# Optimization experiments

Hardware: AMD Instinct MI355X
Metric: run time of the kernel (lower is better)

The kernel has to match this reference:

```python
import jax, jax.numpy as jnp
import numpy as np

D_MODEL = 1024
N_HEAD = 16
D_K = D_MODEL // N_HEAD
D_FF = 2048
EPS = 1e-6
SCALE = np.sqrt(D_K).astype(np.float32)


def layer_norm(x, alpha, beta):
    # Faithful to source: unbiased std (ddof=1), eps added to std
    mean = jnp.mean(x, axis=-1, keepdims=True)
    std = jnp.std(x, axis=-1, keepdims=True, ddof=1) + EPS
    return alpha * (x - mean) / std + beta


def setup_inputs() -> dict:
    key = jax.random.key(0)
    ks = jax.random.split(key, 12)
    s = 0.02
    return {
        "x": jax.random.normal(ks[0], (4, 1024, D_MODEL), dtype=jnp.float32),
        "Wq": jax.random.normal(ks[1], (D_MODEL, D_MODEL), dtype=jnp.float32) * s,
        "bq": jax.random.normal(ks[2], (D_MODEL,), dtype=jnp.float32) * s,
        "Wo": jax.random.normal(ks[3], (D_MODEL, D_MODEL), dtype=jnp.float32) * s,
        "bo": jax.random.normal(ks[4], (D_MODEL,), dtype=jnp.float32) * s,
        "W1": jax.random.normal(ks[5], (D_MODEL, D_FF), dtype=jnp.float32) * s,
        "b1": jax.random.normal(ks[6], (D_FF,), dtype=jnp.float32) * s,
        "W2": jax.random.normal(ks[7], (D_FF, D_MODEL), dtype=jnp.float32) * s,
        "b2": jax.random.normal(ks[8], (D_MODEL,), dtype=jnp.float32) * s,
        "alpha": jnp.ones((D_MODEL,), dtype=jnp.float32),
        "beta": jnp.ones((D_MODEL,), dtype=jnp.float32),
    }


def reference(x, Wq, bq, Wo, bo, W1, b1, W2, b2, alpha, beta):
    b, s, d = x.shape
    # Source bug kept: q, k, v all use q_linear
    def proj(t):
        return (t @ Wq + bq).reshape(b, s, N_HEAD, D_K).transpose(0, 2, 1, 3)
    q = proj(x)  # [b,h,s,dk]
    k = proj(x)
    v = proj(x)
    scores = jnp.einsum('bhqd,bhkd->bhqk', q, k) / SCALE
    scores = jax.nn.softmax(scores, axis=-1)
    z = jnp.einsum('bhqk,bhkd->bhqd', scores, v)
    concat = z.transpose(0, 2, 1, 3).reshape(b, s, d)
    attn_out = concat @ Wo + bo
    x = layer_norm(x + attn_out, alpha, beta)
    ff = jax.nn.relu(x @ W1 + b1) @ W2 + b2
    x = layer_norm(x + ff, alpha, beta)  # source reuses norm_1
    return x
```

## Files before the change

kernel.cpp:

```cpp
#include <hip/hip_runtime.h>
#include <hip/hip_bf16.h>
#include <stdint.h>

#define TOK   4096
#define DMODEL 1024
#define DFF    2048
#define NHEAD  16
#define DK     64

typedef unsigned short u16;
typedef __attribute__((ext_vector_type(8))) short short8;
typedef __attribute__((ext_vector_type(4))) float f32x4;

typedef __attribute__((address_space(1))) void gvoid;
typedef __attribute__((address_space(3))) void lvoid;

#define QSCALE   0.35355339f
#define QUNSCALE 2.82842712f

__device__ __forceinline__ u16 f2b(float f) {
    uint32_t x = __builtin_bit_cast(uint32_t, f);
    x += 0x7FFFu + ((x >> 16) & 1u);
    return (u16)(x >> 16);
}
__device__ __forceinline__ float b2f(u16 u) {
    uint32_t x = ((uint32_t)u) << 16;
    return __builtin_bit_cast(float, x);
}
__device__ __forceinline__ uint32_t f2b2(float lo, float hi) {
    return (uint32_t)f2b(lo) | ((uint32_t)f2b(hi) << 16);
}

__device__ __forceinline__ void gload16(const void* g, void* l) {
    __builtin_amdgcn_global_load_lds((gvoid*)g, (lvoid*)l, 16, 0, 0);
}

__device__ __forceinline__ void cvt_tr_dev(
    const float* __restrict__ W, u16* __restrict__ Wt, int K, int N,
    int bx, int by, int tid, u16 T[64][68])
{
    const int tx = tid & 15, ty = tid >> 4;
    const int n0 = bx * 64, k0 = by * 64;
#pragma unroll
    for (int i = 0; i < 4; i++) {
        int k = ty + i * 16;
        float4 v = *(const float4*)&W[(size_t)(k0 + k) * N + n0 + tx * 4];
        T[tx * 4 + 0][k] = f2b(v.x);
        T[tx * 4 + 1][k] = f2b(v.y);
        T[tx * 4 + 2][k] = f2b(v.z);
        T[tx * 4 + 3][k] = f2b(v.w);
    }
    __syncthreads();
#pragma unroll
    for (int i = 0; i < 4; i++) {
        int n = ty + i * 16;
        ushort4 o;
        o.x = T[n][tx * 4 + 0]; o.y = T[n][tx * 4 + 1];
        o.z = T[n][tx * 4 + 2]; o.w = T[n][tx * 4 + 3];
        *(ushort4*)&Wt[(size_t)(n0 + n) * K + k0 + tx * 4] = o;
    }
}

__global__ __launch_bounds__(256) void prep_all(
    const float* __restrict__ Wq, const float* __restrict__ Wo,
    const float* __restrict__ W1, const float* __restrict__ W2,
    u16* __restrict__ Wqt, u16* __restrict__ Wot,
    u16* __restrict__ W1t, u16* __restrict__ W2t,
    const float* __restrict__ x, u16* __restrict__ xb)
{
    __shared__ u16 T[64][68];
    const int id = blockIdx.x, tid = threadIdx.x;
    if (id < 256) {
        cvt_tr_dev(Wq, Wqt, 1024, 1024, id & 15, id >> 4, tid, T);
    } else if (id < 512) {
        int t = id - 256;
        cvt_tr_dev(Wo, Wot, 1024, 1024, t & 15, t >> 4, tid, T);
    } else if (id < 1024) {
        int t = id - 512;
        cvt_tr_dev(W1, W1t, 1024, 2048, t & 31, t >> 5, tid, T);
    } else if (id < 1536) {
        int t = id - 1024;
        cvt_tr_dev(W2, W2t, 2048, 1024, t & 15, t >> 4, tid, T);
    } else {
        size_t base = (size_t)(id - 1536) * 1024 + tid;
#pragma unroll
        for (int j = 0; j < 4; j++) {
            float4 v = ((const float4*)x)[base + j * 256];
            ((uint2*)xb)[base + j * 256] =
                make_uint2(f2b2(v.x, v.y), f2b2(v.z, v.w));
        }
    }
}

template<int BM, int BN, bool RELU, bool OUTBF16, bool QOUT>
__global__ __launch_bounds__(256) void gemm_mfma(
    const u16* __restrict__ A, const u16* __restrict__ Bt,
    const float* __restrict__ bias, void* __restrict__ Cv,
    u16* __restrict__ CT, float oscale,
    int M, int N, int K)
{
    constexpr int MF = BM / 32;
    constexpr int NF = BN / 32;
    constexpr int ASTR = BM * 64;
    constexpr int BSTR = BN * 64;
    static_assert(MF + NF == 6, "vmcnt immediates assume 6 loads/tile");
    __shared__ __align__(16) u16 As[2 * ASTR];
    __shared__ __align__(16) u16 Bs[2 * BSTR];

    const int tid  = threadIdx.x;
    const int lane = tid & 63;
    const int wid  = tid >> 6;
    const int wm = wid >> 1, wn = wid & 1;
    const int frow = lane & 15, fk = lane >> 4;

    const int gx = N / BN;
    const int gy = M / BM;
    const int rpx = gy >> 3;
    const int L = blockIdx.x;
    const int xcd = L & 7, within = L >> 3;
    const int yy = xcd * rpx + within / gx;
    const int xx = within % gx;

    const int row0 = yy * BM;
    const int col0 = xx * BN;

    const u16* gA[MF]; u16* lA[MF];
    const u16* gB[NF]; u16* lB[NF];
#pragma unroll
    for (int inst = 0; inst < MF; inst++) {
        int s = inst * 256 + tid;
        int r = s >> 3;
        int kc = ((s & 7) ^ (r & 7)) * 8;
        gA[inst] = A + (size_t)(row0 + r) * K + kc;
        lA[inst] = As + inst * 2048 + wid * 512;
    }
#pragma unroll
    for (int inst = 0; inst < NF; inst++) {
        int s = inst * 256 + tid;
        int r = s >> 3;
        int kc = ((s & 7) ^ (r & 7)) * 8;
        gB[inst] = Bt + (size_t)(col0 + r) * K + kc;
        lB[inst] = Bs + inst * 2048 + wid * 512;
    }

    int aoff[MF][2], boff[NF][2];
#pragma unroll
    for (int m = 0; m < MF; m++) {
        int r = wm * (BM / 2) + m * 16 + frow;
#pragma unroll
        for (int kk = 0; kk < 2; kk++)
            aoff[m][kk] = r * 64 + (((kk << 2) + fk) ^ (r & 7)) * 8;
    }
#pragma unroll
    for (int n = 0; n < NF; n++) {
        int r = wn * (BN / 2) + n * 16 + frow;
#pragma unroll
        for (int kk = 0; kk < 2; kk++)
            boff[n][kk] = r * 64 + (((kk << 2) + fk) ^ (r & 7)) * 8;
    }

    f32x4 acc[MF][NF] = {};
    const int nT = K >> 6;

#pragma unroll
    for (int inst = 0; inst < MF; inst++) gload16(gA[inst], lA[inst]);
#pragma unroll
    for (int inst = 0; inst < NF; inst++) gload16(gB[inst], lB[inst]);
#pragma unroll
    for (int inst = 0; inst < MF; inst++) gload16(gA[inst] + 64, lA[inst] + ASTR);
#pragma unroll
    for (int inst = 0; inst < NF; inst++) gload16(gB[inst] + 64, lB[inst] + BSTR);
    asm volatile("s_waitcnt vmcnt(6)" ::: "memory");
    __builtin_amdgcn_sched_barrier(0);
    __builtin_amdgcn_s_barrier();
    __builtin_amdgcn_sched_barrier(0);

    for (int t = 0; t < nT; t++) {
        const int cur = t & 1;
        const u16* Ab = As + cur * ASTR;
        const u16* Bb = Bs + cur * BSTR;
        short8 a[MF][2], b[NF][2];
#pragma unroll
        for (int m = 0; m < MF; m++)
#pragma unroll
            for (int kk = 0; kk < 2; kk++)
                a[m][kk] = *(const short8*)(Ab + aoff[m][kk]);
#pragma unroll
        for (int n = 0; n < NF; n++)
#pragma unroll
            for (int kk = 0; kk < 2; kk++)
                b[n][kk] = *(const short8*)(Bb + boff[n][kk]);

#pragma unroll
        for (int m = 0; m < MF; m++)
#pragma unroll
            for (int n = 0; n < NF; n++)
#pragma unroll
                for (int kk = 0; kk < 2; kk++)
                    acc[m][n] = __builtin_amdgcn_mfma_f32_16x16x32_bf16(
                        a[m][kk], b[n][kk], acc[m][n], 0, 0, 0);

        __builtin_amdgcn_sched_barrier(0);
        __builtin_amdgcn_s_barrier();
        __builtin_amdgcn_sched_barrier(0);

        if (t + 2 < nT) {
            const int k0 = (t + 2) << 6;
#pragma unroll
            for (int inst = 0; inst < MF; inst++)
                gload16(gA[inst] + k0, lA[inst] + cur * ASTR);
#pragma unroll
            for (int inst = 0; inst < NF; inst++)
                gload16(gB[inst] + k0, lB[inst] + cur * BSTR);
        }
        if (t + 1 < nT) {
            if (t + 2 < nT) asm volatile("s_waitcnt vmcnt(6)" ::: "memory");
            else            asm volatile("s_waitcnt vmcnt(0)" ::: "memory");
            __builtin_amdgcn_sched_barrier(0);
            __builtin_amdgcn_s_barrier();
            __builtin_amdgcn_sched_barrier(0);
        }
    }

#pragma unroll
    for (int n = 0; n < NF; n++) {
        const int gcol = col0 + wn * (BN / 2) + n * 16 + frow;
        const float bv = bias[gcol];
#pragma unroll
        for (int m = 0; m < MF; m++) {
            const int grow0 = row0 + wm * (BM / 2) + m * 16 + fk * 4;
            float v[4];
#pragma unroll
            for (int i = 0; i < 4; i++) {
                v[i] = (acc[m][n][i] + bv) * oscale;
                if (RELU) v[i] = fmaxf(v[i], 0.0f);
                if (OUTBF16)
                    ((u16*)Cv)[(size_t)(grow0 + i) * N + gcol] = f2b(v[i]);
                else
                    ((float*)Cv)[(size_t)(grow0 + i) * N + gcol] = v[i];
            }
            if (QOUT) {
                const int hh = gcol >> 6, d = gcol & 63;
                const int bb = grow0 >> 10, sl = grow0 & 1023;
                *(uint2*)&CT[(((size_t)(bb * 16 + hh) * 64 + d) << 10) + sl] =
                    make_uint2(f2b2(v[0], v[1]), f2b2(v[2], v[3]));
            }
        }
    }
}

__global__ __launch_bounds__(256, 2) void attn_mfma(
    const u16* __restrict__ qb, const u16* __restrict__ qT,
    u16* __restrict__ zb)
{
    __shared__ __align__(16) u16 Ks[2][64 * 64];
    __shared__ __align__(16) u16 Kt[2][64 * 64];
    __shared__ __align__(16) u16 Ps[128 * 64];

    const int tid  = threadIdx.x;
    const int lane = tid & 63;
    const int w    = tid >> 6;
    const int frow = lane & 15, fk = lane >> 4;

    const int h  = blockIdx.x;
    const int qt = blockIdx.y;
    const int b  = blockIdx.z;
    const int q0 = qt * 128;

    const u16* qhead = qb + ((size_t)b * 1024) * 1024 + h * 64;
    const u16* thead = qT + ((size_t)(b * 16 + h) * 64) * 1024;

#pragma unroll
    for (int inst = 0; inst < 2; inst++) {
        int s = inst * 256 + tid, r = s >> 3, kc = ((s & 7) ^ (r & 7)) * 8;
        gload16(qhead + (size_t)r * 1024 + kc, Ks[0] + inst * 2048 + w * 512);
        gload16(thead + (size_t)r * 1024 + kc, Kt[0] + inst * 2048 + w * 512);
    }

    short8 qf[2][2];
#pragma unroll
    for (int m = 0; m < 2; m++) {
        int r = q0 + w * 32 + m * 16 + frow;
#pragma unroll
        for (int kk = 0; kk < 2; kk++)
            qf[m][kk] = *(const short8*)(qhead + (size_t)r * 1024 + kk * 32 + fk * 8);
    }

    float lp[2] = {};
    f32x4 o[2][4] = {};

    __syncthreads();

    for (int t = 0; t < 16; t++) {
        const int cur = t & 1;
        if (t < 15) {
            const int kv = (t + 1) * 64;
#pragma unroll
            for (int inst = 0; inst < 2; inst++) {
                int s = inst * 256 + tid, r = s >> 3, kc = ((s & 7) ^ (r & 7)) * 8;
                gload16(qhead + (size_t)(kv + r) * 1024 + kc,
                        Ks[cur ^ 1] + inst * 2048 + w * 512);
                gload16(thead + (size_t)r * 1024 + kv + kc,
                        Kt[cur ^ 1] + inst * 2048 + w * 512);
            }
        }

        short8 kf[4][2];
#pragma unroll
        for (int n = 0; n < 4; n++) {
            int r = n * 16 + frow;
#pragma unroll
            for (int kk = 0; kk < 2; kk++)
                kf[n][kk] = *(const short8*)(Ks[cur] + r * 64 +
                                             (((kk << 2) + fk) ^ (r & 7)) * 8);
        }
        f32x4 st[4][2] = {};
#pragma unroll
        for (int nk = 0; nk < 4; nk++)
#pragma unroll
            for (int mq = 0; mq < 2; mq++)
#pragma unroll
                for (int kk = 0; kk < 2; kk++)
                    st[nk][mq] = __builtin_amdgcn_mfma_f32_16x16x32_bf16(
                        kf[nk][kk], qf[mq][kk], st[nk][mq], 0, 0, 0);

#pragma unroll
        for (int mq = 0; mq < 2; mq++) {
            const int r = w * 32 + mq * 16 + frow;
            const int rb = r * 64, sw = (r & 7) << 3;
#pragma unroll
            for (int nk = 0; nk < 4; nk++) {
                float p0 = __expf(st[nk][mq][0]);
                float p1 = __expf(st[nk][mq][1]);
                float p2 = __expf(st[nk][mq][2]);
                float p3 = __expf(st[nk][mq][3]);
                lp[mq] += (p0 + p1) + (p2 + p3);
                *(uint2*)&Ps[rb + ((nk * 16 + fk * 4) ^ sw)] =
                    make_uint2(f2b2(p0, p1), f2b2(p2, p3));
            }
        }

        short8 pa[2][2], vf[4][2];
#pragma unroll
        for (int m = 0; m < 2; m++) {
            int r = w * 32 + m * 16 + frow;
#pragma unroll
            for (int kk = 0; kk < 2; kk++)
                pa[m][kk] = *(const short8*)(Ps + r * 64 +
                                             (((kk << 2) + fk) ^ (r & 7)) * 8);
        }
#pragma unroll
        for (int n = 0; n < 4; n++) {
            int r = n * 16 + frow;
#pragma unroll
            for (int kk = 0; kk < 2; kk++)
                vf[n][kk] = *(const short8*)(Kt[cur] + r * 64 +
                                             (((kk << 2) + fk) ^ (r & 7)) * 8);
        }
#pragma unroll
        for (int m = 0; m < 2; m++)
#pragma unroll
            for (int n = 0; n < 4; n++)
#pragma unroll
                for (int kk = 0; kk < 2; kk++)
                    o[m][n] = __builtin_amdgcn_mfma_f32_16x16x32_bf16(
                        pa[m][kk], vf[n][kk], o[m][n], 0, 0, 0);

        __syncthreads();
    }

#pragma unroll
    for (int mq = 0; mq < 2; mq++) {
        lp[mq] += __shfl_xor(lp[mq], 16);
        lp[mq] += __shfl_xor(lp[mq], 32);
    }
#pragma unroll
    for (int m = 0; m < 2; m++)
#pragma unroll
        for (int i = 0; i < 4; i++) {
            const float lfull = __shfl(lp[m], fk * 4 + i);
            const float rl = QUNSCALE / lfull;
            const size_t gr = (size_t)(b * 1024 + q0 + w * 32 + m * 16 + fk * 4 + i);
#pragma unroll
            for (int n = 0; n < 4; n++)
                zb[gr * 1024 + h * 64 + n * 16 + frow] = f2b(o[m][n][i] * rl);
        }
}

__device__ __forceinline__ float4 ld4(const float* p) { return *(const float4*)p; }
__device__ __forceinline__ float4 ld4(const u16* p) {
    ushort4 u = *(const ushort4*)p;
    return make_float4(b2f(u.x), b2f(u.y), b2f(u.z), b2f(u.w));
}
__device__ __forceinline__ void st4(float* p, float4 v) { *(float4*)p = v; }
__device__ __forceinline__ void st4(u16* p, float4 v) {
    *(uint2*)p = make_uint2(f2b2(v.x, v.y), f2b2(v.z, v.w));
}

template<typename TA, typename TB, typename TO>
__global__ __launch_bounds__(256) void add_ln(
    const TA* __restrict__ a, const TB* __restrict__ b,
    const float* __restrict__ alpha, const float* __restrict__ beta,
    TO* __restrict__ out)
{
    const int row = blockIdx.x;
    const int c = threadIdx.x * 4;
    float4 va = ld4(a + (size_t)row * DMODEL + c);
    float4 vb = ld4(b + (size_t)row * DMODEL + c);
    float v0 = va.x + vb.x, v1 = va.y + vb.y;
    float v2 = va.z + vb.z, v3 = va.w + vb.w;

    float sum = (v0 + v1) + (v2 + v3);
    float sq  = (v0 * v0 + v1 * v1) + (v2 * v2 + v3 * v3);
#pragma unroll
    for (int off = 32; off > 0; off >>= 1) {
        sum += __shfl_xor(sum, off);
        sq  += __shfl_xor(sq, off);
    }
    __shared__ float s1[4], s2[4];
    const int wid = threadIdx.x >> 6, lane = threadIdx.x & 63;
    if (lane == 0) { s1[wid] = sum; s2[wid] = sq; }
    __syncthreads();
    sum = (s1[0] + s1[1]) + (s1[2] + s1[3]);
    sq  = (s2[0] + s2[1]) + (s2[2] + s2[3]);

    const float mean = sum * (1.0f / 1024.0f);
    float var = (sq - 1024.0f * mean * mean) * (1.0f / 1023.0f);
    var = fmaxf(var, 0.0f);
    const float rdenom = 1.0f / (sqrtf(var) + 1e-6f);

    float4 al = *(const float4*)(alpha + c);
    float4 be = *(const float4*)(beta + c);
    float4 r;
    r.x = al.x * (v0 - mean) * rdenom + be.x;
    r.y = al.y * (v1 - mean) * rdenom + be.y;
    r.z = al.z * (v2 - mean) * rdenom + be.z;
    r.w = al.w * (v3 - mean) * rdenom + be.w;
    st4(out + (size_t)row * DMODEL + c, r);
}

extern "C" void kernel_launch(void* const* d_in, const int* in_sizes, int n_in,
                              void* d_out, int out_size, void* d_ws, size_t ws_size,
                              hipStream_t stream) {
    const float* x     = (const float*)d_in[0];
    const float* Wq    = (const float*)d_in[1];
    const float* bq    = (const float*)d_in[2];
    const float* Wo    = (const float*)d_in[3];
    const float* bo    = (const float*)d_in[4];
    const float* W1    = (const float*)d_in[5];
    const float* b1    = (const float*)d_in[6];
    const float* W2    = (const float*)d_in[7];
    const float* b2    = (const float*)d_in[8];
    const float* alpha = (const float*)d_in[9];
    const float* beta  = (const float*)d_in[10];

    char* base = (char*)d_ws;
    u16* Wqt = (u16*)base;
    u16* Wot = (u16*)(base + (2u  << 20));
    u16* W1t = (u16*)(base + (4u  << 20));
    u16* W2t = (u16*)(base + (8u  << 20));
    u16* zb  = (u16*)(base + (12u << 20));
    u16* x1b = zb;
    u16* qb  = (u16*)(base + (20u << 20));
    u16* g2  = qb;
    u16* qT  = (u16*)(base + (28u << 20));
    u16* xb  = (u16*)(base + (36u << 20));
    u16* g   = xb;
    u16* hb  = (u16*)(base + (36u << 20));

    dim3 blk(256);

    prep_all<<<dim3(2560), blk, 0, stream>>>(
        Wq, Wo, W1, W2, Wqt, Wot, W1t, W2t, x, xb);

    gemm_mfma<128, 64, false, true, true><<<dim3(512), blk, 0, stream>>>(
        xb, Wqt, bq, qb, qT, QSCALE, TOK, 1024, 1024);
    attn_mfma<<<dim3(16, 8, 4), blk, 0, stream>>>(qb, qT, zb);
    gemm_mfma<128, 64, false, true, false><<<dim3(512), blk, 0, stream>>>(
        zb, Wot, bo, g, nullptr, 1.0f, TOK, 1024, 1024);
    add_ln<float, u16, u16><<<dim3(TOK), blk, 0, stream>>>(x, g, alpha, beta, x1b);
    gemm_mfma<128, 64, true, true, false><<<dim3(1024), blk, 0, stream>>>(
        x1b, W1t, b1, hb, nullptr, 1.0f, TOK, 2048, 1024);
    gemm_mfma<128, 64, false, true, false><<<dim3(512), blk, 0, stream>>>(
        hb, W2t, b2, g2, nullptr, 1.0f, TOK, 1024, 2048);
    add_ln<u16, u16, float><<<dim3(TOK), blk, 0, stream>>>(
        x1b, g2, alpha, beta, (float*)d_out);
}
```

Baseline: 149.7 us.

## Overlap weight conversion with attention and shrink GEMM tiles for more blocks

Splits the weight prep so only Wq and x are converted before the Q projection, and the Wo/W1/W2 transpose-conversions run as extra blocks inside the attention kernel launch, reusing its LDS. The GEMMs switch to 64x64 (and 64x128 for FFN1) tiles, doubling block counts to improve CU occupancy and load balance. The vmcnt waits are generalised to the per-tile load count. Smaller tiles reduce data reuse per block, and the merged attention launch may see its attention blocks contend with the conversion blocks.

```diff
diff --git a/kernel.cpp b/kernel.cpp
--- a/kernel.cpp
+++ b/kernel.cpp
@@ -35,9 +35,16 @@
     __builtin_amdgcn_global_load_lds((gvoid*)g, (lvoid*)l, 16, 0, 0);
 }
 
+template<int N>
+__device__ __forceinline__ void wait_vm() {
+    if constexpr (N == 0) asm volatile("s_waitcnt vmcnt(0)" ::: "memory");
+    else if constexpr (N == 4) asm volatile("s_waitcnt vmcnt(4)" ::: "memory");
+    else if constexpr (N == 6) asm volatile("s_waitcnt vmcnt(6)" ::: "memory");
+}
+
 __device__ __forceinline__ void cvt_tr_dev(
     const float* __restrict__ W, u16* __restrict__ Wt, int K, int N,
-    int bx, int by, int tid, u16 T[64][68])
+    int bx, int by, int tid, u16 (*T)[68])
 {
     const int tx = tid & 15, ty = tid >> 4;
     const int n0 = bx * 64, k0 = by * 64;
@@ -61,28 +68,16 @@
     }
 }
 
-__global__ __launch_bounds__(256) void prep_all(
-    const float* __restrict__ Wq, const float* __restrict__ Wo,
-    const float* __restrict__ W1, const float* __restrict__ W2,
-    u16* __restrict__ Wqt, u16* __restrict__ Wot,
-    u16* __restrict__ W1t, u16* __restrict__ W2t,
+__global__ __launch_bounds__(256) void prep1(
+    const float* __restrict__ Wq, u16* __restrict__ Wqt,
     const float* __restrict__ x, u16* __restrict__ xb)
 {
     __shared__ u16 T[64][68];
     const int id = blockIdx.x, tid = threadIdx.x;
     if (id < 256) {
         cvt_tr_dev(Wq, Wqt, 1024, 1024, id & 15, id >> 4, tid, T);
-    } else if (id < 512) {
-        int t = id - 256;
-        cvt_tr_dev(Wo, Wot, 1024, 1024, t & 15, t >> 4, tid, T);
-    } else if (id < 1024) {
-        int t = id - 512;
-        cvt_tr_dev(W1, W1t, 1024, 2048, t & 31, t >> 5, tid, T);
-    } else if (id < 1536) {
-        int t = id - 1024;
-        cvt_tr_dev(W2, W2t, 2048, 1024, t & 15, t >> 4, tid, T);
     } else {
-        size_t base = (size_t)(id - 1536) * 1024 + tid;
+        size_t base = (size_t)(id - 256) * 1024 + tid;
 #pragma unroll
         for (int j = 0; j < 4; j++) {
             float4 v = ((const float4*)x)[base + j * 256];
@@ -101,9 +96,9 @@
 {
     constexpr int MF = BM / 32;
     constexpr int NF = BN / 32;
+    constexpr int LD = MF + NF;
     constexpr int ASTR = BM * 64;
     constexpr int BSTR = BN * 64;
-    static_assert(MF + NF == 6, "vmcnt immediates assume 6 loads/tile");
     __shared__ __align__(16) u16 As[2 * ASTR];
     __shared__ __align__(16) u16 Bs[2 * BSTR];
 
@@ -170,7 +165,7 @@
     for (int inst = 0; inst < MF; inst++) gload16(gA[inst] + 64, lA[inst] + ASTR);
 #pragma unroll
     for (int inst = 0; inst < NF; inst++) gload16(gB[inst] + 64, lB[inst] + BSTR);
-    asm volatile("s_waitcnt vmcnt(6)" ::: "memory");
+    wait_vm<LD>();
     __builtin_amdgcn_sched_barrier(0);
     __builtin_amdgcn_s_barrier();
     __builtin_amdgcn_sched_barrier(0);
@@ -214,8 +209,8 @@
                 gload16(gB[inst] + k0, lB[inst] + cur * BSTR);
         }
         if (t + 1 < nT) {
-            if (t + 2 < nT) asm volatile("s_waitcnt vmcnt(6)" ::: "memory");
-            else            asm volatile("s_waitcnt vmcnt(0)" ::: "memory");
+            if (t + 2 < nT) wait_vm<LD>();
+            else            wait_vm<0>();
             __builtin_amdgcn_sched_barrier(0);
             __builtin_amdgcn_s_barrier();
             __builtin_amdgcn_sched_barrier(0);
@@ -249,22 +244,36 @@
     }
 }
 
-__global__ __launch_bounds__(256, 2) void attn_mfma(
+__global__ __launch_bounds__(256, 2) void attn_prepw(
     const u16* __restrict__ qb, const u16* __restrict__ qT,
-    u16* __restrict__ zb)
+    u16* __restrict__ zb,
+    const float* __restrict__ Wo, const float* __restrict__ W1,
+    const float* __restrict__ W2,
+    u16* __restrict__ Wot, u16* __restrict__ W1t, u16* __restrict__ W2t)
 {
     __shared__ __align__(16) u16 Ks[2][64 * 64];
     __shared__ __align__(16) u16 Kt[2][64 * 64];
     __shared__ __align__(16) u16 Ps[128 * 64];
 
-    const int tid  = threadIdx.x;
+    const int tid = threadIdx.x;
+    const int id  = blockIdx.x;
+
+    if (id >= 512) {
+        u16 (*T)[68] = reinterpret_cast<u16 (*)[68]>(&Ks[0][0]);
+        int t = id - 512;
+        if (t < 256)       cvt_tr_dev(Wo, Wot, 1024, 1024, t & 15, t >> 4, tid, T);
+        else if (t < 768)  { t -= 256; cvt_tr_dev(W1, W1t, 1024, 2048, t & 31, t >> 5, tid, T); }
+        else               { t -= 768; cvt_tr_dev(W2, W2t, 2048, 1024, t & 15, t >> 4, tid, T); }
+        return;
+    }
+
     const int lane = tid & 63;
     const int w    = tid >> 6;
     const int frow = lane & 15, fk = lane >> 4;
 
-    const int h  = blockIdx.x;
-    const int qt = blockIdx.y;
-    const int b  = blockIdx.z;
+    const int h  = id & 15;
+    const int qt = (id >> 4) & 7;
+    const int b  = id >> 7;
     const int q0 = qt * 128;
 
     const u16* qhead = qb + ((size_t)b * 1024) * 1024 + h * 64;
@@ -470,18 +479,18 @@
 
     dim3 blk(256);
 
-    prep_all<<<dim3(2560), blk, 0, stream>>>(
-        Wq, Wo, W1, W2, Wqt, Wot, W1t, W2t, x, xb);
-
-    gemm_mfma<128, 64, false, true, true><<<dim3(512), blk, 0, stream>>>(
+    prep1<<<dim3(1280), blk, 0, stream>>>(Wq, Wqt, x, xb);
+
+    gemm_mfma<64, 64, false, true, true><<<dim3(1024), blk, 0, stream>>>(
         xb, Wqt, bq, qb, qT, QSCALE, TOK, 1024, 1024);
-    attn_mfma<<<dim3(16, 8, 4), blk, 0, stream>>>(qb, qT, zb);
-    gemm_mfma<128, 64, false, true, false><<<dim3(512), blk, 0, stream>>>(
+    attn_prepw<<<dim3(1792), blk, 0, stream>>>(
+        qb, qT, zb, Wo, W1, W2, Wot, W1t, W2t);
+    gemm_mfma<64, 64, false, true, false><<<dim3(1024), blk, 0, stream>>>(
         zb, Wot, bo, g, nullptr, 1.0f, TOK, 1024, 1024);
     add_ln<float, u16, u16><<<dim3(TOK), blk, 0, stream>>>(x, g, alpha, beta, x1b);
-    gemm_mfma<128, 64, true, true, false><<<dim3(1024), blk, 0, stream>>>(
+    gemm_mfma<64, 128, true, true, false><<<dim3(1024), blk, 0, stream>>>(
         x1b, W1t, b1, hb, nullptr, 1.0f, TOK, 2048, 1024);
-    gemm_mfma<128, 64, false, true, false><<<dim3(512), blk, 0, stream>>>(
+    gemm_mfma<64, 64, false, true, false><<<dim3(1024), blk, 0, stream>>>(
         hb, W2t, b2, g2, nullptr, 1.0f, TOK, 1024, 2048);
     add_ln<u16, u16, float><<<dim3(TOK), blk, 0, stream>>>(
         x1b, g2, alpha, beta, (float*)d_out);
```

New measurement: 143.4 us. 4.2% less time.
